# Performance work log

Measured on AMD Instinct MI355X. Metric: run time of the kernel, lower is better.

The kernel has to match this reference:

```python
import jax, jax.numpy as jnp
import numpy as np
from jax import lax

R = 1.0                 # object_bounding_sphere
SDF_THR = 5e-05
LINE_SEARCH_STEP = 0.5
LINE_STEP_ITERS = 1
SPHERE_TRACING_ITERS = 10
N_STEPS = 100
N_SECANT = 8
B, P = 4, 32768


def _sdf(p, center, radius):
    # analytic sphere SDF standing in for the opaque external sdf network
    return jnp.sqrt(jnp.sum((p - center) ** 2, axis=-1) + 1e-12) - radius[0]


def setup_inputs() -> dict:
    key = jax.random.key(0)
    k1, k2, k3 = jax.random.split(key, 3)
    cd = jax.random.normal(k1, (B, 3), dtype=jnp.float32)
    cam_loc = 2.5 * cd / jnp.linalg.norm(cd, axis=-1, keepdims=True)  # cameras outside bounding sphere
    d = -cam_loc[:, None, :] + 0.5 * jax.random.normal(k2, (B, P, 3), dtype=jnp.float32)
    ray_directions = d / jnp.linalg.norm(d, axis=-1, keepdims=True)   # rays aimed near origin
    object_mask = jax.random.bernoulli(k3, 0.5, (B * P,))
    sdf_center = jnp.array([0.1, -0.05, 0.08], dtype=jnp.float32)
    sdf_radius = jnp.array([0.7], dtype=jnp.float32)
    return {"cam_loc": cam_loc, "ray_directions": ray_directions,
            "object_mask": object_mask, "sdf_center": sdf_center, "sdf_radius": sdf_radius}


def _safe_div(a, b):
    return a / jnp.where(b == 0, 1.0, b)


def _forward(cam_loc, ray_directions, sdf_center, sdf_radius):
    sdf = lambda p: _sdf(p, sdf_center, sdf_radius)
    b, p, _ = ray_directions.shape
    n = b * p
    dirs = ray_directions.reshape(n, 3)
    cam = jnp.broadcast_to(cam_loc[:, None, :], (b, p, 3)).reshape(n, 3)

    # ---- sphere intersection with bounding sphere of radius R ----
    ray_cam_dot = jnp.einsum('nd,nd->n', dirs, cam)
    under_sqrt = ray_cam_dot ** 2 - (jnp.sum(cam ** 2, axis=-1) - R ** 2)
    mask_intersect = under_sqrt > 0
    sq = jnp.sqrt(jnp.where(mask_intersect, under_sqrt, 0.0))
    si = jnp.stack([-sq - ray_cam_dot, sq - ray_cam_dot], axis=-1)   # [N,2] near/far distances
    si = jnp.maximum(jnp.where(mask_intersect[:, None], si, 0.0), 0.0)

    # ---- sphere tracing (fixed trip count; masked lanes are no-ops, matching the torch early-break) ----
    acc_s = jnp.where(mask_intersect, si[:, 0], 0.0)
    acc_e = jnp.where(mask_intersect, si[:, 1], 0.0)
    pts_s = jnp.where(mask_intersect[:, None], cam + acc_s[:, None] * dirs, 0.0)
    pts_e = jnp.where(mask_intersect[:, None], cam + acc_e[:, None] * dirs, 0.0)
    next_s = jnp.where(mask_intersect, sdf(pts_s), 0.0)
    next_e = jnp.where(mask_intersect, sdf(pts_e), 0.0)

    def body(i, st):
        unfin_s, unfin_e, acc_s, acc_e, next_s, next_e, pts_s, pts_e = st
        curr_s = jnp.where(unfin_s, next_s, 0.0)
        curr_s = jnp.where(curr_s <= SDF_THR, 0.0, curr_s)
        curr_e = jnp.where(unfin_e, next_e, 0.0)
        curr_e = jnp.where(curr_e <= SDF_THR, 0.0, curr_e)
        unfin_s = unfin_s & (curr_s > SDF_THR)
        unfin_e = unfin_e & (curr_e > SDF_THR)
        acc_s = acc_s + curr_s
        acc_e = acc_e - curr_e
        pts_s = cam + acc_s[:, None] * dirs
        pts_e = cam + acc_e[:, None] * dirs
        next_s = jnp.where(unfin_s, sdf(pts_s), 0.0)
        next_e = jnp.where(unfin_e, sdf(pts_e), 0.0)
        # line search back-off for overshoot (line_step_iters fixed small)
        for j in range(LINE_STEP_ITERS):
            step = (1.0 - LINE_SEARCH_STEP) / (2.0 ** j)
            np_s = next_s < 0
            np_e = next_e < 0
            acc_s = jnp.where(np_s, acc_s - step * curr_s, acc_s)
            acc_e = jnp.where(np_e, acc_e + step * curr_e, acc_e)
            pts_s = jnp.where(np_s[:, None], cam + acc_s[:, None] * dirs, pts_s)
            pts_e = jnp.where(np_e[:, None], cam + acc_e[:, None] * dirs, pts_e)
            next_s = jnp.where(np_s, sdf(pts_s), next_s)
            next_e = jnp.where(np_e, sdf(pts_e), next_e)
        ok = acc_s < acc_e
        return (unfin_s & ok, unfin_e & ok, acc_s, acc_e, next_s, next_e, pts_s, pts_e)

    st = (mask_intersect, mask_intersect, acc_s, acc_e, next_s, next_e, pts_s, pts_e)
    unfin_s, unfin_e, acc_s, acc_e, next_s, next_e, pts_s, pts_e = lax.fori_loop(
        0, SPHERE_TRACING_ITERS, body, st)
    # final mask refresh (the break iteration of the torch while-loop)
    curr_s = jnp.where(unfin_s, next_s, 0.0)
    curr_s = jnp.where(curr_s <= SDF_THR, 0.0, curr_s)
    unfin_s = unfin_s & (curr_s > SDF_THR)

    network_object_mask = acc_s < acc_e
    sampler_mask = unfin_s

    # ---- ray sampler: dense march along unconverged rays ----
    smin = jnp.where(sampler_mask, acc_s, 0.0)
    smax = jnp.where(sampler_mask, acc_e, 0.0)
    t = jnp.linspace(0.0, 1.0, N_STEPS)
    z = smin[:, None] + t[None, :] * (smax - smin)[:, None]          # [N,S]
    pts = cam[:, None, :] + z[..., None] * dirs[:, None, :]          # [N,S,3]
    sdf_val = sdf(pts)                                               # [N,S]
    # first index where sign flips to negative (IDR trick)
    tmp = jnp.sign(sdf_val) * jnp.arange(N_STEPS, 0, -1, dtype=sdf_val.dtype)
    ind = jnp.argmin(tmp, axis=-1)
    row = jnp.arange(n)
    z_high = z[row, ind]
    sdf_high = sdf_val[row, ind]
    p_ind = pts[row, ind]
    net_surface = sdf_high < 0
    z_low = z[row, ind - 1]      # ind==0 wraps, same as torch -1 indexing
    sdf_low = sdf_val[row, ind - 1]

    # ---- secant root finding ----
    z_pred = -sdf_low * _safe_div(z_high - z_low, sdf_high - sdf_low) + z_low

    def sec_body(i, st):
        z_low, z_high, sdf_low, sdf_high, z_pred = st
        sdf_mid = sdf(cam + z_pred[:, None] * dirs)
        low_m = sdf_mid > 0
        high_m = sdf_mid < 0
        z_low = jnp.where(low_m, z_pred, z_low)
        sdf_low = jnp.where(low_m, sdf_mid, sdf_low)
        z_high = jnp.where(high_m, z_pred, z_high)
        sdf_high = jnp.where(high_m, sdf_mid, sdf_high)
        z_pred = -sdf_low * _safe_div(z_high - z_low, sdf_high - sdf_low) + z_low
        return (z_low, z_high, sdf_low, sdf_high, z_pred)

    _, _, _, _, z_pred = lax.fori_loop(0, N_SECANT, sec_body,
                                       (z_low, z_high, sdf_low, sdf_high, z_pred))

    secant_mask = sampler_mask & net_surface
    sampler_pts = jnp.where(secant_mask[:, None], cam + z_pred[:, None] * dirs, p_ind)
    sampler_dists = jnp.where(secant_mask, z_pred, z_high)
    sampler_net_obj_mask = sampler_mask & net_surface

    curr_start_points = jnp.where(sampler_mask[:, None], sampler_pts, pts_s)
    acc_start_dis = jnp.where(sampler_mask, sampler_dists, acc_s)
    network_object_mask = jnp.where(sampler_mask, sampler_net_obj_mask, network_object_mask)
    return curr_start_points, network_object_mask, acc_start_dis


def reference(cam_loc, ray_directions, object_mask, sdf_center, sdf_radius):
    # eval-mode forward: object_mask only affects the training-only tail of torch forward
    return _forward(cam_loc, ray_directions, sdf_center, sdf_radius)
```

## Files before the change

### kernel.cpp

```cpp
#include <hip/hip_runtime.h>


#define PP        32768
#define SDF_THR   5e-05f
#define NSTEPS    100
#define NSECANT   8
#define NTRACE    10

__device__ __forceinline__ float fsqrt(float x) {
    float r; asm("v_sqrt_f32 %0, %1" : "=v"(r) : "v"(x)); return r;
}
__device__ __forceinline__ float frcp(float x) {
    float r; asm("v_rcp_f32 %0, %1" : "=v"(r) : "v"(x)); return r;
}

__global__ __launch_bounds__(256) void ray_trace_kernel(
    const float* __restrict__ cam_loc,
    const float* __restrict__ ray_dirs,
    const float* __restrict__ sdf_center,
    const float* __restrict__ sdf_radius,
    float* __restrict__ out,
    int n_total)
{
    int t = blockIdx.x * blockDim.x + threadIdx.x;
    int n = t >> 1;
    int h = t & 1;
    if (n >= n_total) return;
    int b = n >> 15;

    const float dx = ray_dirs[3*n+0], dy = ray_dirs[3*n+1], dz = ray_dirs[3*n+2];
    const float cx = cam_loc[3*b+0], cy = cam_loc[3*b+1], cz = cam_loc[3*b+2];
    const float scx = sdf_center[0], scy = sdf_center[1], scz = sdf_center[2];
    const float rad = sdf_radius[0];

    const float ex = cx - scx, ey = cy - scy, ez = cz - scz;
    const float dd  = dx*dx + dy*dy + dz*dz;
    const float de2 = 2.0f * (dx*ex + dy*ey + dz*ez);
    const float ee1 = (ex*ex + ey*ey + ez*ez) + 1e-12f;

    float rcd  = dx*cx + dy*cy + dz*cz;
    float cam2 = cx*cx + cy*cy + cz*cz;
    float under = rcd*rcd - (cam2 - 1.0f);
    bool mask_int = under > 0.0f;
    float sq = fsqrt(mask_int ? under : 0.0f);
    float si0 = fmaxf(mask_int ? (-sq - rcd) : 0.0f, 0.0f);
    float si1 = fmaxf(mask_int ? ( sq - rcd) : 0.0f, 0.0f);

    float my_acc = h ? si1 : si0;
    const float sgn = h ? -1.0f : 1.0f;
    bool my_unfin = mask_int;
    {
        float u0 = fmaf(my_acc, fmaf(my_acc, dd, de2), ee1);
        float nv = fsqrt(u0) - rad;
        my_acc = my_acc;
        (void)nv;
    }
    float next;
    {
        float u0 = fmaf(my_acc, fmaf(my_acc, dd, de2), ee1);
        next = my_unfin ? (fsqrt(u0) - rad) : 0.0f;
    }

    float acc_s = my_acc, acc_e = my_acc;
    #pragma unroll
    for (int it = 0; it < NTRACE; ++it) {
        float curr = my_unfin ? next : 0.0f;
        curr = (curr <= SDF_THR) ? 0.0f : curr;
        my_unfin = my_unfin && (curr > SDF_THR);
        my_acc = fmaf(sgn, curr, my_acc);
        float u = fmaf(my_acc, fmaf(my_acc, dd, de2), ee1);
        next = my_unfin ? (fsqrt(u) - rad) : 0.0f;
        if (next < 0.0f) {
            my_acc = fmaf(-sgn, 0.5f * curr, my_acc);
            float u2 = fmaf(my_acc, fmaf(my_acc, dd, de2), ee1);
            next = fsqrt(u2) - rad;
        }
        float pacc = __shfl_xor(my_acc, 1);
        acc_s = h ? pacc : my_acc;
        acc_e = h ? my_acc : pacc;
        bool ok = acc_s < acc_e;
        my_unfin = my_unfin && ok;
    }
    bool unfin_s_f = my_unfin;
    {
        float curr = my_unfin ? next : 0.0f;
        curr = (curr <= SDF_THR) ? 0.0f : curr;
        unfin_s_f = my_unfin && (curr > SDF_THR);
    }
    int smi = __shfl_xor(h ? 0 : (int)unfin_s_f, 1);
    const bool sampler = h ? (smi != 0) : unfin_s_f;
    const bool netmask_trace = acc_s < acc_e;

    bool net_surface = false;
    float z_pred = 0.0f, zh_out = 0.0f;
    float pix = 0.0f, piy = 0.0f, piz = 0.0f;

    if (__ballot(sampler) != 0ULL) {
        float smin = sampler ? acc_s : 0.0f;
        float smax = sampler ? acc_e : 0.0f;
        float sz = (smax - smin) * (1.0f / 99.0f);

        float r2 = rad * rad;
        unsigned rb = __float_as_uint(r2);
        float u_neg_max = __uint_as_float(rb - 7u);
        float u_le_max  = u_neg_max;
        #pragma unroll
        for (int k = -6; k <= 6; ++k) {
            float u = __uint_as_float(rb + (unsigned)k);
            float v = fsqrt(u);
            if (v <  rad) u_neg_max = u;
            if (v <= rad) u_le_max  = u;
        }

        float kmf = 1e30f;
        float i_f = (float)h;
        #pragma unroll
        for (int s = 0; s < NSTEPS / 2; ++s) {
            float z = fmaf(i_f, sz, smin);
            float u = fmaf(z, fmaf(z, dd, de2), ee1);
            float cand = (u <= u_le_max) ? i_f : 1e30f;
            kmf = fminf(kmf, cand);
            i_f += 2.0f;
        }
        kmf = fminf(kmf, __shfl_xor(kmf, 1));

        int ind;
        if (kmf < 1e29f) {
            int km = (int)kmf;
            float zk = fmaf(kmf, sz, smin);
            float uk = fmaf(zk, fmaf(zk, dd, de2), ee1);
            if (uk <= u_neg_max) {
                ind = km; net_surface = true;
            } else {
                ind = km; net_surface = false;
                for (int i = km + 1; i < NSTEPS; ++i) {
                    float z = fmaf((float)i, sz, smin);
                    float u = fmaf(z, fmaf(z, dd, de2), ee1);
                    if (u <= u_neg_max) { ind = i; net_surface = true; break; }
                }
            }
        } else {
            ind = NSTEPS - 1; net_surface = false;
        }
        int indm1 = (ind == 0) ? (NSTEPS - 1) : (ind - 1);

        float z_high = fmaf((float)ind,   sz, smin);
        float z_low  = fmaf((float)indm1, sz, smin);
        zh_out = z_high;
        float uh = fmaf(z_high, fmaf(z_high, dd, de2), ee1);
        float ul = fmaf(z_low,  fmaf(z_low,  dd, de2), ee1);
        float sdf_high = fsqrt(uh) - rad;
        float sdf_low  = fsqrt(ul) - rad;
        pix = fmaf(z_high, dx, cx);
        piy = fmaf(z_high, dy, cy);
        piz = fmaf(z_high, dz, cz);

        float den = sdf_high - sdf_low;
        float dinv = frcp((den == 0.0f) ? 1.0f : den);
        z_pred = fmaf(-sdf_low, (z_high - z_low) * dinv, z_low);
        #pragma unroll
        for (int i = 0; i < NSECANT; ++i) {
            float um = fmaf(z_pred, fmaf(z_pred, dd, de2), ee1);
            float sm = fsqrt(um) - rad;
            if (sm > 0.0f) { z_low  = z_pred; sdf_low  = sm; }
            if (sm < 0.0f) { z_high = z_pred; sdf_high = sm; }
            den = sdf_high - sdf_low;
            dinv = frcp((den == 0.0f) ? 1.0f : den);
            z_pred = fmaf(-sdf_low, (z_high - z_low) * dinv, z_low);
        }
    }

    float ox, oy, oz, odis;
    bool omask;
    if (sampler) {
        if (net_surface) {
            ox = fmaf(z_pred, dx, cx);
            oy = fmaf(z_pred, dy, cy);
            oz = fmaf(z_pred, dz, cz);
            odis = z_pred;
        } else {
            ox = pix; oy = piy; oz = piz;
            odis = zh_out;
        }
        omask = net_surface;
    } else {
        ox = fmaf(acc_s, dx, cx);
        oy = fmaf(acc_s, dy, cy);
        oz = fmaf(acc_s, dz, cz);
        odis = acc_s;
        omask = netmask_trace;
    }

    if (h == 0) {
        out[3*n + 0] = ox;
        out[3*n + 1] = oy;
        out[3*n + 2] = oz;
    } else {
        out[3*n_total + n] = omask ? 1.0f : 0.0f;
        out[4*n_total + n] = odis;
    }
}

extern "C" void kernel_launch(void* const* d_in, const int* in_sizes, int n_in,
                              void* d_out, int out_size, void* d_ws, size_t ws_size,
                              hipStream_t stream) {
    const float* cam_loc    = (const float*)d_in[0];
    const float* ray_dirs   = (const float*)d_in[1];
    const float* sdf_center = (const float*)d_in[3];
    const float* sdf_radius = (const float*)d_in[4];
    float* out = (float*)d_out;

    int n_total = in_sizes[1] / 3;
    int threads = 2 * n_total;
    int block = 256;
    int grid = (threads + block - 1) / block;
    ray_trace_kernel<<<grid, block, 0, stream>>>(cam_loc, ray_dirs, sdf_center,
                                                 sdf_radius, out, n_total);
}
```

Measured before the change: 12.18 us.

## Compact sampler rays in shared memory and process each with four lanes

After sphere tracing, rays still needing the sampler phase are compacted per block into shared memory with ballot/popcount prefix sums. Each compacted ray is then handled by four lanes that split the 100-step linear search, instead of the original divergent pair layout where whole wavefronts ran the sampler when any lane needed it. Non-sampler rays write their outputs early. The change adds two block barriers and shared-memory traffic, and re-loads ray data for the compacted rays.

Result: slower. 16.33 us (+34.0%).

```diff
diff --git a/kernel.cpp b/kernel.cpp
--- a/kernel.cpp
+++ b/kernel.cpp
@@ -1,7 +1,6 @@
 #include <hip/hip_runtime.h>
 
 
-#define PP        32768
 #define SDF_THR   5e-05f
 #define NSTEPS    100
 #define NSECANT   8
@@ -14,7 +13,7 @@
     float r; asm("v_rcp_f32 %0, %1" : "=v"(r) : "v"(x)); return r;
 }
 
-__global__ __launch_bounds__(256) void ray_trace_kernel(
+__global__ __launch_bounds__(256) void ray_kernel(
     const float* __restrict__ cam_loc,
     const float* __restrict__ ray_dirs,
     const float* __restrict__ sdf_center,
@@ -22,13 +21,18 @@
     float* __restrict__ out,
     int n_total)
 {
-    int t = blockIdx.x * blockDim.x + threadIdx.x;
-    int n = t >> 1;
-    int h = t & 1;
-    if (n >= n_total) return;
-    int b = n >> 15;
-
-    const float dx = ray_dirs[3*n+0], dy = ray_dirs[3*n+1], dz = ray_dirs[3*n+2];
+    __shared__ unsigned short s_idx[128];
+    __shared__ float2         s_mm[128];
+    __shared__ unsigned       s_wcnt[4];
+
+    const int t = blockIdx.x * blockDim.x + threadIdx.x;
+    const int n = t >> 1;
+    const int h = t & 1;
+    const bool valid = (n < n_total);
+    const int nc = valid ? n : 0;
+    const int b = nc >> 15;
+
+    const float dx = ray_dirs[3*nc+0], dy = ray_dirs[3*nc+1], dz = ray_dirs[3*nc+2];
     const float cx = cam_loc[3*b+0], cy = cam_loc[3*b+1], cz = cam_loc[3*b+2];
     const float scx = sdf_center[0], scy = sdf_center[1], scz = sdf_center[2];
     const float rad = sdf_radius[0];
@@ -41,7 +45,7 @@
     float rcd  = dx*cx + dy*cy + dz*cz;
     float cam2 = cx*cx + cy*cy + cz*cz;
     float under = rcd*rcd - (cam2 - 1.0f);
-    bool mask_int = under > 0.0f;
+    bool mask_int = valid && (under > 0.0f);
     float sq = fsqrt(mask_int ? under : 0.0f);
     float si0 = fmaxf(mask_int ? (-sq - rcd) : 0.0f, 0.0f);
     float si1 = fmaxf(mask_int ? ( sq - rcd) : 0.0f, 0.0f);
@@ -49,12 +53,6 @@
     float my_acc = h ? si1 : si0;
     const float sgn = h ? -1.0f : 1.0f;
     bool my_unfin = mask_int;
-    {
-        float u0 = fmaf(my_acc, fmaf(my_acc, dd, de2), ee1);
-        float nv = fsqrt(u0) - rad;
-        my_acc = my_acc;
-        (void)nv;
-    }
     float next;
     {
         float u0 = fmaf(my_acc, fmaf(my_acc, dd, de2), ee1);
@@ -81,61 +79,104 @@
         bool ok = acc_s < acc_e;
         my_unfin = my_unfin && ok;
     }
-    bool unfin_s_f = my_unfin;
+    bool sampler_s = my_unfin;
     {
         float curr = my_unfin ? next : 0.0f;
         curr = (curr <= SDF_THR) ? 0.0f : curr;
-        unfin_s_f = my_unfin && (curr > SDF_THR);
-    }
-    int smi = __shfl_xor(h ? 0 : (int)unfin_s_f, 1);
-    const bool sampler = h ? (smi != 0) : unfin_s_f;
+        sampler_s = my_unfin && (curr > SDF_THR);
+    }
     const bool netmask_trace = acc_s < acc_e;
 
-    bool net_surface = false;
-    float z_pred = 0.0f, zh_out = 0.0f;
-    float pix = 0.0f, piy = 0.0f, piz = 0.0f;
-
-    if (__ballot(sampler) != 0ULL) {
-        float smin = sampler ? acc_s : 0.0f;
-        float smax = sampler ? acc_e : 0.0f;
-        float sz = (smax - smin) * (1.0f / 99.0f);
-
-        float r2 = rad * rad;
-        unsigned rb = __float_as_uint(r2);
-        float u_neg_max = __uint_as_float(rb - 7u);
-        float u_le_max  = u_neg_max;
+    int smi = __shfl_xor(h ? 0 : (int)sampler_s, 1);
+    const bool sampler = h ? (smi != 0) : sampler_s;
+
+    if (valid && !sampler) {
+        if (h == 0) {
+            out[3*n + 0] = fmaf(acc_s, dx, cx);
+            out[3*n + 1] = fmaf(acc_s, dy, cy);
+            out[3*n + 2] = fmaf(acc_s, dz, cz);
+        } else {
+            out[3*n_total + n] = netmask_trace ? 1.0f : 0.0f;
+            out[4*n_total + n] = acc_s;
+        }
+    }
+
+    bool want = valid && (h == 0) && sampler_s;
+    unsigned long long m = __ballot(want);
+    const int wid  = threadIdx.x >> 6;
+    const int lane = threadIdx.x & 63;
+    if (lane == 0) s_wcnt[wid] = (unsigned)__popcll(m);
+    __syncthreads();
+    unsigned base = 0;
+    #pragma unroll
+    for (int w = 0; w < 3; ++w) if (w < wid) base += s_wcnt[w];
+    const unsigned total = s_wcnt[0] + s_wcnt[1] + s_wcnt[2] + s_wcnt[3];
+    if (want) {
+        unsigned pos = base + (unsigned)__popcll(m & ((1ULL << lane) - 1ULL));
+        s_idx[pos] = (unsigned short)(threadIdx.x >> 1);
+        s_mm[pos]  = make_float2(acc_s, acc_e);
+    }
+    __syncthreads();
+
+    if (total == 0) return;
+
+    float r2 = rad * rad;
+    unsigned rb = __float_as_uint(r2);
+    float u_neg_max = __uint_as_float(rb - 7u);
+    float u_le_max  = u_neg_max;
+    #pragma unroll
+    for (int k = -6; k <= 6; ++k) {
+        float u = __uint_as_float(rb + (unsigned)k);
+        float v = fsqrt(u);
+        if (v <  rad) u_neg_max = u;
+        if (v <= rad) u_le_max  = u;
+    }
+
+    const int slot0 = threadIdx.x >> 2;
+    const int q = threadIdx.x & 3;
+    const int ray_base = (blockIdx.x * blockDim.x) >> 1;
+
+    for (unsigned slot = (unsigned)slot0; slot < total; slot += 64) {
+        const int r = (int)s_idx[slot];
+        const float2 mm = s_mm[slot];
+        const float smin = mm.x, smax = mm.y;
+        const int nn = ray_base + r;
+        const int bb = nn >> 15;
+
+        const float rdx = ray_dirs[3*nn+0], rdy = ray_dirs[3*nn+1], rdz = ray_dirs[3*nn+2];
+        const float rcx = cam_loc[3*bb+0], rcy = cam_loc[3*bb+1], rcz = cam_loc[3*bb+2];
+        const float rex = rcx - scx, rey = rcy - scy, rez = rcz - scz;
+        const float rdd  = rdx*rdx + rdy*rdy + rdz*rdz;
+        const float rde2 = 2.0f * (rdx*rex + rdy*rey + rdz*rez);
+        const float ree1 = (rex*rex + rey*rey + rez*rez) + 1e-12f;
+
+        const float sz = (smax - smin) * (1.0f / 99.0f);
+
+        float kmf = 1e30f;
+        float i_f = (float)q;
         #pragma unroll
-        for (int k = -6; k <= 6; ++k) {
-            float u = __uint_as_float(rb + (unsigned)k);
-            float v = fsqrt(u);
-            if (v <  rad) u_neg_max = u;
-            if (v <= rad) u_le_max  = u;
-        }
-
-        float kmf = 1e30f;
-        float i_f = (float)h;
-        #pragma unroll
-        for (int s = 0; s < NSTEPS / 2; ++s) {
+        for (int s = 0; s < NSTEPS / 4; ++s) {
             float z = fmaf(i_f, sz, smin);
-            float u = fmaf(z, fmaf(z, dd, de2), ee1);
-            float cand = (u <= u_le_max) ? i_f : 1e30f;
-            kmf = fminf(kmf, cand);
-            i_f += 2.0f;
+            float u = fmaf(z, fmaf(z, rdd, rde2), ree1);
+            kmf = fminf(kmf, (u <= u_le_max) ? i_f : 1e30f);
+            i_f += 4.0f;
         }
         kmf = fminf(kmf, __shfl_xor(kmf, 1));
-
+        kmf = fminf(kmf, __shfl_xor(kmf, 2));
+
+        bool net_surface = false;
         int ind;
         if (kmf < 1e29f) {
             int km = (int)kmf;
             float zk = fmaf(kmf, sz, smin);
-            float uk = fmaf(zk, fmaf(zk, dd, de2), ee1);
+            float uk = fmaf(zk, fmaf(zk, rdd, rde2), ree1);
             if (uk <= u_neg_max) {
                 ind = km; net_surface = true;
             } else {
                 ind = km; net_surface = false;
                 for (int i = km + 1; i < NSTEPS; ++i) {
                     float z = fmaf((float)i, sz, smin);
-                    float u = fmaf(z, fmaf(z, dd, de2), ee1);
+                    float u = fmaf(z, fmaf(z, rdd, rde2), ree1);
                     if (u <= u_neg_max) { ind = i; net_surface = true; break; }
                 }
             }
@@ -146,21 +187,21 @@
 
         float z_high = fmaf((float)ind,   sz, smin);
         float z_low  = fmaf((float)indm1, sz, smin);
-        zh_out = z_high;
-        float uh = fmaf(z_high, fmaf(z_high, dd, de2), ee1);
-        float ul = fmaf(z_low,  fmaf(z_low,  dd, de2), ee1);
+        float zh_out = z_high;
+        float uh = fmaf(z_high, fmaf(z_high, rdd, rde2), ree1);
+        float ul = fmaf(z_low,  fmaf(z_low,  rdd, rde2), ree1);
         float sdf_high = fsqrt(uh) - rad;
         float sdf_low  = fsqrt(ul) - rad;
-        pix = fmaf(z_high, dx, cx);
-        piy = fmaf(z_high, dy, cy);
-        piz = fmaf(z_high, dz, cz);
+        float pix = fmaf(z_high, rdx, rcx);
+        float piy = fmaf(z_high, rdy, rcy);
+        float piz = fmaf(z_high, rdz, rcz);
 
         float den = sdf_high - sdf_low;
         float dinv = frcp((den == 0.0f) ? 1.0f : den);
-        z_pred = fmaf(-sdf_low, (z_high - z_low) * dinv, z_low);
+        float z_pred = fmaf(-sdf_low, (z_high - z_low) * dinv, z_low);
         #pragma unroll
         for (int i = 0; i < NSECANT; ++i) {
-            float um = fmaf(z_pred, fmaf(z_pred, dd, de2), ee1);
+            float um = fmaf(z_pred, fmaf(z_pred, rdd, rde2), ree1);
             float sm = fsqrt(um) - rad;
             if (sm > 0.0f) { z_low  = z_pred; sdf_low  = sm; }
             if (sm < 0.0f) { z_high = z_pred; sdf_high = sm; }
@@ -168,36 +209,26 @@
             dinv = frcp((den == 0.0f) ? 1.0f : den);
             z_pred = fmaf(-sdf_low, (z_high - z_low) * dinv, z_low);
         }
-    }
-
-    float ox, oy, oz, odis;
-    bool omask;
-    if (sampler) {
+
+        float ox, oy, oz, odis;
         if (net_surface) {
-            ox = fmaf(z_pred, dx, cx);
-            oy = fmaf(z_pred, dy, cy);
-            oz = fmaf(z_pred, dz, cz);
+            ox = fmaf(z_pred, rdx, rcx);
+            oy = fmaf(z_pred, rdy, rcy);
+            oz = fmaf(z_pred, rdz, rcz);
             odis = z_pred;
         } else {
             ox = pix; oy = piy; oz = piz;
             odis = zh_out;
         }
-        omask = net_surface;
-    } else {
-        ox = fmaf(acc_s, dx, cx);
-        oy = fmaf(acc_s, dy, cy);
-        oz = fmaf(acc_s, dz, cz);
-        odis = acc_s;
-        omask = netmask_trace;
-    }
-
-    if (h == 0) {
-        out[3*n + 0] = ox;
-        out[3*n + 1] = oy;
-        out[3*n + 2] = oz;
-    } else {
-        out[3*n_total + n] = omask ? 1.0f : 0.0f;
-        out[4*n_total + n] = odis;
+        if (q == 0) {
+            out[3*nn + 0] = ox;
+            out[3*nn + 1] = oy;
+            out[3*nn + 2] = oz;
+        } else if (q == 1) {
+            out[3*n_total + nn] = net_surface ? 1.0f : 0.0f;
+        } else if (q == 2) {
+            out[4*n_total + nn] = odis;
+        }
     }
 }
 
@@ -214,6 +245,6 @@
     int threads = 2 * n_total;
     int block = 256;
     int grid = (threads + block - 1) / block;
-    ray_trace_kernel<<<grid, block, 0, stream>>>(cam_loc, ray_dirs, sdf_center,
-                                                 sdf_radius, out, n_total);
-}
+    ray_kernel<<<grid, block, 0, stream>>>(cam_loc, ray_dirs, sdf_center,
+                                           sdf_radius, out, n_total);
+}
```
